# Kernel tuning notes

Hardware: AMD Instinct MI355X
Metric: run time of the kernel (lower is better)

Reference implementation:

```python
import jax, jax.numpy as jnp
import numpy as np
from jax import lax

MAX_DEG = 10
BATCH = 4096
PER_DEG = 50000              # atoms per degree bucket
N_ATOMS = PER_DEG * (MAX_DEG + 1)
F = 128                      # n_atom_features == nb_filter
EPS = 1e-5


def setup_inputs() -> dict:
    key = jax.random.key(0)
    ks = jax.random.split(key, 8)
    atoms = jax.random.normal(ks[0], (N_ATOMS, F), jnp.float32)
    # atoms sorted by degree: degree d occupies rows [d*PER_DEG, (d+1)*PER_DEG)
    deg_slice = jnp.stack([jnp.arange(MAX_DEG + 1) * PER_DEG,
                           jnp.full((MAX_DEG + 1,), PER_DEG)], axis=1).astype(jnp.int32)
    membership = jax.random.randint(ks[1], (N_ATOMS,), 0, BATCH, dtype=jnp.int32)
    inp = {"atoms": atoms, "deg_slice": deg_slice, "membership": membership}
    for d in range(1, MAX_DEG + 1):
        inp[f"adj_{d}"] = jax.random.randint(jax.random.fold_in(key, d),
                                             (PER_DEG, d), 0, N_ATOMS, dtype=jnp.int32)
    inp["W"] = jax.random.normal(ks[2], (2 * MAX_DEG + 1, F, F), jnp.float32) * 0.05
    inp["b"] = jnp.zeros((2 * MAX_DEG + 1, F), jnp.float32)
    inp["gW"] = jax.random.normal(ks[3], (MAX_DEG + 1, F, F), jnp.float32) * 0.05
    inp["gb"] = jnp.zeros((MAX_DEG + 1, F), jnp.float32)
    inp["gamma"] = jnp.ones((F,), jnp.float32)
    inp["beta"] = jnp.zeros((F,), jnp.float32)
    return inp


def reference(atoms, deg_slice, membership,
              adj_1, adj_2, adj_3, adj_4, adj_5, adj_6, adj_7, adj_8, adj_9, adj_10,
              W, b, gW, gb, gamma, beta):
    adjs = [adj_1, adj_2, adj_3, adj_4, adj_5, adj_6, adj_7, adj_8, adj_9, adj_10]
    rel_outs = [None] * (MAX_DEG + 1)
    gat_outs = [None] * (MAX_DEG + 1)
    for d in range(1, MAX_DEG + 1):
        nbr_sum = jnp.take(atoms, adjs[d - 1], axis=0).sum(axis=1)  # (PER_DEG, F)
        self_atoms = lax.dynamic_slice_in_dim(atoms, deg_slice[d, 0], PER_DEG, axis=0)
        rel_outs[d] = (nbr_sum @ W[2 * (d - 1)] + b[2 * (d - 1)]
                       + self_atoms @ W[2 * (d - 1) + 1] + b[2 * (d - 1) + 1])
        gat_outs[d] = self_atoms @ gW[d - 1] + gb[d - 1]
    # degree 0 (min_deg == 0): self transform only
    self0 = lax.dynamic_slice_in_dim(atoms, deg_slice[0, 0], PER_DEG, axis=0)
    rel_outs[0] = self0 @ W[2 * MAX_DEG] + b[2 * MAX_DEG]
    gat_outs[0] = self0 @ gW[MAX_DEG] + gb[MAX_DEG]

    activated = jnp.concatenate(rel_outs, axis=0)     # (N_ATOMS, F), degree order == atom order
    gather_atoms = jnp.concatenate(gat_outs, axis=0)  # (N_ATOMS, F)
    # graph_gather: per-molecule sum (tf.dynamic_partition + reduce_sum == segment_sum)
    graph_feat = jax.ops.segment_sum(gather_atoms, membership, num_segments=BATCH)
    # activation is 'linear' (identity); layer-norm on atom features as in call()
    m = activated.mean(axis=-1, keepdims=True)
    std = jnp.sqrt(activated.var(axis=-1, keepdims=True) + EPS)
    normed = gamma * ((activated - m) / (std + EPS)) + beta
    return normed, graph_feat
```

## Files before the change

### kernel.cpp

```cpp
#include <hip/hip_runtime.h>
#include <hip/hip_bf16.h>

#define F_DIM   128
#define PER_DEG 50000
#define NDEG    11
#define MAXD    10
#define BATCH   4096
#define N_ATOMS (PER_DEG * NDEG)

#define BM    64
#define LDST  264
#define BPD   ((PER_DEG + BM - 1) / BM)
#define WT_K  384

typedef __attribute__((ext_vector_type(4))) float f32x4;
typedef __attribute__((ext_vector_type(8))) short short8v;
typedef __attribute__((ext_vector_type(4))) short short4v;

struct AdjPtrs { const int* p[MAXD]; };

__device__ inline short bf16bits(float x) {
    __hip_bfloat16 h = __float2bfloat16(x);
    return __builtin_bit_cast(short, h);
}
__device__ inline float bf_lo(unsigned u) {
    return __builtin_bit_cast(float, u << 16);
}
__device__ inline float bf_hi(unsigned u) {
    return __builtin_bit_cast(float, u & 0xFFFF0000u);
}

__global__ void prep_wt(const float* __restrict__ W, const float* __restrict__ gW,
                        short* __restrict__ wt) {
    int idx = blockIdx.x * blockDim.x + threadIdx.x;
    const int total = NDEG * F_DIM * WT_K;
    if (idx >= total) return;
    int d   = idx / (F_DIM * WT_K);
    int rem = idx % (F_DIM * WT_K);
    int c   = rem / WT_K;
    int k   = rem % WT_K;
    float v;
    if (k < 256) {
        if (d == 0) {
            v = (k < 128) ? 0.0f : W[20 * 16384 + (k - 128) * F_DIM + c];
        } else {
            int wi = (k < 128) ? (2 * (d - 1)) : (2 * (d - 1) + 1);
            v = W[wi * 16384 + (k & 127) * F_DIM + c];
        }
    } else {
        int gidx = (d == 0) ? 10 : (d - 1);
        v = gW[gidx * 16384 + (k - 256) * F_DIM + c];
    }
    wt[idx] = bf16bits(v);
}

__global__ void to_bf16(const float* __restrict__ in, short* __restrict__ out) {
    const size_t n8 = (size_t)N_ATOMS * F_DIM / 8;
    size_t stride = (size_t)gridDim.x * blockDim.x;
    for (size_t k = (size_t)blockIdx.x * blockDim.x + threadIdx.x; k < n8; k += stride) {
        f32x4 a = ((const f32x4*)in)[2 * k];
        f32x4 c = ((const f32x4*)in)[2 * k + 1];
        short8v o = { bf16bits(a[0]), bf16bits(a[1]), bf16bits(a[2]), bf16bits(a[3]),
                      bf16bits(c[0]), bf16bits(c[1]), bf16bits(c[2]), bf16bits(c[3]) };
        ((short8v*)out)[k] = o;
    }
}

template<int GBF>
__global__ __launch_bounds__(256, 2) void fused_gc(
    const float* __restrict__ atoms,
    const short* __restrict__ abf,
    const int*   __restrict__ membership,
    AdjPtrs adj,
    const short* __restrict__ wt,
    const float* __restrict__ b,
    const float* __restrict__ gb,
    const float* __restrict__ gamma,
    const float* __restrict__ beta,
    float* __restrict__ outN,
    float* __restrict__ outG)
{
    __shared__ short As[BM * LDST];
    const int bid   = blockIdx.x;
    const int d     = bid / BPD;
    const int rb    = bid % BPD;
    const int rows0 = rb * BM;
    const int tid   = threadIdx.x;

    {
        const int rloc = tid >> 2;
        const int p    = tid & 3;
        const int grow = rows0 + rloc;
        const bool rv  = grow < PER_DEG;
        short* basep = &As[rloc * LDST + p * 32];

        if (GBF) {
            float acc[32];
            #pragma unroll
            for (int e = 0; e < 32; ++e) acc[e] = 0.0f;
            if (rv && d > 0) {
                const int* ar = adj.p[d - 1] + (size_t)grow * d;
                int idxs[MAXD];
                #pragma unroll
                for (int j = 0; j < MAXD; ++j) idxs[j] = (j < d) ? ar[j] : 0;
                #pragma unroll
                for (int j = 0; j < MAXD; ++j) {
                    if (j < d) {
                        const uint4* s = (const uint4*)(abf + (size_t)idxs[j] * F_DIM) + p * 4;
                        #pragma unroll
                        for (int q = 0; q < 4; ++q) {
                            uint4 u = s[q];
                            acc[q * 8 + 0] += bf_lo(u.x); acc[q * 8 + 1] += bf_hi(u.x);
                            acc[q * 8 + 2] += bf_lo(u.y); acc[q * 8 + 3] += bf_hi(u.y);
                            acc[q * 8 + 4] += bf_lo(u.z); acc[q * 8 + 5] += bf_hi(u.z);
                            acc[q * 8 + 6] += bf_lo(u.w); acc[q * 8 + 7] += bf_hi(u.w);
                        }
                    }
                }
            }
            #pragma unroll
            for (int q = 0; q < 4; ++q) {
                short8v nb = { bf16bits(acc[q * 8 + 0]), bf16bits(acc[q * 8 + 1]),
                               bf16bits(acc[q * 8 + 2]), bf16bits(acc[q * 8 + 3]),
                               bf16bits(acc[q * 8 + 4]), bf16bits(acc[q * 8 + 5]),
                               bf16bits(acc[q * 8 + 6]), bf16bits(acc[q * 8 + 7]) };
                *(short8v*)(basep + q * 8) = nb;
            }
            const uint4* ss = (const uint4*)(abf + (size_t)(d * PER_DEG + grow) * F_DIM) + p * 4;
            uint4 z = {0u, 0u, 0u, 0u};
            #pragma unroll
            for (int q = 0; q < 4; ++q)
                *(uint4*)(basep + 128 + q * 8) = rv ? ss[q] : z;
        } else {
            f32x4 accn[8], selfv[8];
            #pragma unroll
            for (int q = 0; q < 8; ++q) { accn[q] = 0.0f; selfv[q] = 0.0f; }
            const f32x4* atomsv = (const f32x4*)atoms;
            if (rv) {
                if (d > 0) {
                    const int* ar = adj.p[d - 1] + (size_t)grow * d;
                    int idxs[MAXD];
                    #pragma unroll
                    for (int j = 0; j < MAXD; ++j) idxs[j] = (j < d) ? ar[j] : 0;
                    #pragma unroll
                    for (int j = 0; j < MAXD; ++j) {
                        if (j < d) {
                            const f32x4* s = atomsv + (size_t)idxs[j] * 32 + p * 8;
                            #pragma unroll
                            for (int q = 0; q < 8; ++q) accn[q] += s[q];
                        }
                    }
                }
                const f32x4* s = atomsv + (size_t)(d * PER_DEG + grow) * 32 + p * 8;
                #pragma unroll
                for (int q = 0; q < 8; ++q) selfv[q] = s[q];
            }
            #pragma unroll
            for (int q = 0; q < 8; ++q) {
                short4v nb = { bf16bits(accn[q][0]),  bf16bits(accn[q][1]),
                               bf16bits(accn[q][2]),  bf16bits(accn[q][3]) };
                short4v sv = { bf16bits(selfv[q][0]), bf16bits(selfv[q][1]),
                               bf16bits(selfv[q][2]), bf16bits(selfv[q][3]) };
                *(short4v*)(basep + q * 4)       = nb;
                *(short4v*)(basep + 128 + q * 4) = sv;
            }
        }
    }
    __syncthreads();

    const int w  = tid >> 6;
    const int l  = tid & 63;
    const int cg = l & 15;
    const int rg = l >> 4;

    short8v a[8];
    const short* arow = &As[(w * 16 + cg) * LDST + rg * 8];
    #pragma unroll
    for (int s = 0; s < 8; ++s) a[s] = *(const short8v*)(arow + s * 32);

    const short* wtd = wt + (size_t)d * F_DIM * WT_K;
    f32x4 aA[8], aG[8];
    #pragma unroll
    for (int n = 0; n < 8; ++n) { aA[n] = 0.0f; aG[n] = 0.0f; }

    #pragma unroll
    for (int s = 0; s < 8; ++s) {
        #pragma unroll
        for (int n = 0; n < 8; ++n) {
            short8v bv = *(const short8v*)(wtd + (n * 16 + cg) * WT_K + s * 32 + rg * 8);
            aA[n] = __builtin_amdgcn_mfma_f32_16x16x32_bf16(a[s], bv, aA[n], 0, 0, 0);
        }
    }
    #pragma unroll
    for (int s = 0; s < 4; ++s) {
        #pragma unroll
        for (int n = 0; n < 8; ++n) {
            short8v bv = *(const short8v*)(wtd + (n * 16 + cg) * WT_K + 256 + s * 32 + rg * 8);
            aG[n] = __builtin_amdgcn_mfma_f32_16x16x32_bf16(a[4 + s], bv, aG[n], 0, 0, 0);
        }
    }

    const int gidx = (d == 0) ? 10 : (d - 1);
    float biasv[8], gbv[8], gam[8], bet[8];
    #pragma unroll
    for (int n = 0; n < 8; ++n) {
        int col = n * 16 + cg;
        biasv[n] = (d > 0) ? (b[(2 * d - 2) * F_DIM + col] + b[(2 * d - 1) * F_DIM + col])
                           : b[20 * F_DIM + col];
        gbv[n] = gb[gidx * F_DIM + col];
        gam[n] = gamma[col];
        bet[n] = beta[col];
    }
    const int valid = (PER_DEG - rows0 < BM) ? (PER_DEG - rows0) : BM;
    #pragma unroll
    for (int j = 0; j < 4; ++j) {
        const int rl = w * 16 + rg * 4 + j;
        float x[8];
        float s1 = 0.f, s2 = 0.f;
        #pragma unroll
        for (int n = 0; n < 8; ++n) {
            x[n] = aA[n][j] + biasv[n];
            s1 += x[n];
            s2 += x[n] * x[n];
        }
        #pragma unroll
        for (int m = 1; m < 16; m <<= 1) {
            s1 += __shfl_xor(s1, m);
            s2 += __shfl_xor(s2, m);
        }
        float mean = s1 * (1.0f / 128.0f);
        float var  = fmaxf(s2 * (1.0f / 128.0f) - mean * mean, 0.0f);
        float inv  = 1.0f / (sqrtf(var + 1e-5f) + 1e-5f);
        if (rl < valid) {
            const int growi = d * PER_DEG + rows0 + rl;
            float* op = outN + (size_t)growi * F_DIM;
            float* gp = outG + (size_t)membership[growi] * F_DIM;
            #pragma unroll
            for (int n = 0; n < 8; ++n) {
                int col = n * 16 + cg;
                op[col] = gam[n] * ((x[n] - mean) * inv) + bet[n];
                atomicAdd(&gp[col], aG[n][j] + gbv[n]);
            }
        }
    }
}

extern "C" void kernel_launch(void* const* d_in, const int* in_sizes, int n_in,
                              void* d_out, int out_size, void* d_ws, size_t ws_size,
                              hipStream_t stream) {
    const float* atoms      = (const float*)d_in[0];
    const int*   membership = (const int*)d_in[2];
    AdjPtrs adj;
    for (int i = 0; i < MAXD; ++i) adj.p[i] = (const int*)d_in[3 + i];
    const float* W     = (const float*)d_in[13];
    const float* b     = (const float*)d_in[14];
    const float* gW    = (const float*)d_in[15];
    const float* gb    = (const float*)d_in[16];
    const float* gamma = (const float*)d_in[17];
    const float* beta  = (const float*)d_in[18];

    float* outN = (float*)d_out;
    float* outG = outN + (size_t)N_ATOMS * F_DIM;

    const size_t wt_bytes  = (size_t)NDEG * F_DIM * WT_K * sizeof(short);
    const size_t abf_off   = (wt_bytes + 255) & ~(size_t)255;
    const size_t abf_bytes = (size_t)N_ATOMS * F_DIM * sizeof(short);
    const bool use_bf16 = ws_size >= abf_off + abf_bytes;

    short* wt = (short*)d_ws;
    const int prep_total = NDEG * F_DIM * WT_K;
    prep_wt<<<(prep_total + 255) / 256, 256, 0, stream>>>(W, gW, wt);
    hipMemsetAsync(outG, 0, (size_t)BATCH * F_DIM * sizeof(float), stream);

    if (use_bf16) {
        short* abf = (short*)((char*)d_ws + abf_off);
        to_bf16<<<2048, 256, 0, stream>>>(atoms, abf);
        fused_gc<1><<<NDEG * BPD, 256, 0, stream>>>(atoms, abf, membership, adj, wt,
                                                    b, gb, gamma, beta, outN, outG);
    } else {
        fused_gc<0><<<NDEG * BPD, 256, 0, stream>>>(atoms, nullptr, membership, adj, wt,
                                                    b, gb, gamma, beta, outN, outG);
    }
}
```

Before: 737.0 us.

## Replace per-atom gather GEMM and atomics with per-molecule sum then small GEMM

Uses linearity to move the graph gather past the matrix multiply. Atom features are first summed per (molecule, degree) bucket, using a histogram, scan and scatter to group atom indices. A small GEMM over the 1440-wide concatenated sums, with bias folded in via counts, then produces the molecule features. This removes the per-atom gather matmul and the 64M float atomicAdds from the main kernel, which now needs less LDS and targets higher occupancy. In exchange it adds several small kernels and a serial per-molecule reduction loop.

Result: faster. 619.9 us (-15.9%).

```diff
diff --git a/kernel.cpp b/kernel.cpp
--- a/kernel.cpp
+++ b/kernel.cpp
@@ -8,10 +8,13 @@
 #define BATCH   4096
 #define N_ATOMS (PER_DEG * NDEG)
 
-#define BM    64
-#define LDST  264
-#define BPD   ((PER_DEG + BM - 1) / BM)
-#define WT_K  384
+#define BM     64
+#define LDSN   136
+#define BPD    ((PER_DEG + BM - 1) / BM)
+#define WT_K   256
+#define GWT_K  1440
+#define LDST_L 264
+#define WT_K_L 384
 
 typedef __attribute__((ext_vector_type(4))) float f32x4;
 typedef __attribute__((ext_vector_type(8))) short short8v;
@@ -23,15 +26,13 @@
     __hip_bfloat16 h = __float2bfloat16(x);
     return __builtin_bit_cast(short, h);
 }
-__device__ inline float bf_lo(unsigned u) {
-    return __builtin_bit_cast(float, u << 16);
-}
-__device__ inline float bf_hi(unsigned u) {
-    return __builtin_bit_cast(float, u & 0xFFFF0000u);
-}
-
-__global__ void prep_wt(const float* __restrict__ W, const float* __restrict__ gW,
-                        short* __restrict__ wt) {
+__device__ inline float bf_lo(unsigned u) { return __builtin_bit_cast(float, u << 16); }
+__device__ inline float bf_hi(unsigned u) { return __builtin_bit_cast(float, u & 0xFFFF0000u); }
+__device__ inline float bf2f(short s) {
+    return __builtin_bit_cast(float, ((unsigned)(unsigned short)s) << 16);
+}
+
+__global__ void prep_wt_main(const float* __restrict__ W, short* __restrict__ wt) {
     int idx = blockIdx.x * blockDim.x + threadIdx.x;
     const int total = NDEG * F_DIM * WT_K;
     if (idx >= total) return;
@@ -40,18 +41,33 @@
     int c   = rem / WT_K;
     int k   = rem % WT_K;
     float v;
-    if (k < 256) {
-        if (d == 0) {
-            v = (k < 128) ? 0.0f : W[20 * 16384 + (k - 128) * F_DIM + c];
-        } else {
-            int wi = (k < 128) ? (2 * (d - 1)) : (2 * (d - 1) + 1);
-            v = W[wi * 16384 + (k & 127) * F_DIM + c];
-        }
+    if (d == 0) {
+        v = (k < 128) ? 0.0f : W[20 * 16384 + (k - 128) * F_DIM + c];
     } else {
-        int gidx = (d == 0) ? 10 : (d - 1);
-        v = gW[gidx * 16384 + (k - 256) * F_DIM + c];
+        int wi = (k < 128) ? (2 * (d - 1)) : (2 * (d - 1) + 1);
+        v = W[wi * 16384 + (k & 127) * F_DIM + c];
     }
     wt[idx] = bf16bits(v);
+}
+
+__global__ void prep_gwt(const float* __restrict__ gW, const float* __restrict__ gb,
+                         short* __restrict__ gwt) {
+    int idx = blockIdx.x * blockDim.x + threadIdx.x;
+    const int total = F_DIM * GWT_K;
+    if (idx >= total) return;
+    int c = idx / GWT_K;
+    int k = idx % GWT_K;
+    float v = 0.0f;
+    if (k < 1408) {
+        int dd = k >> 7, f = k & 127;
+        int gi = dd ? (dd - 1) : 10;
+        v = gW[gi * 16384 + f * F_DIM + c];
+    } else if (k < 1419) {
+        int dd = k - 1408;
+        int gi = dd ? (dd - 1) : 10;
+        v = gb[gi * F_DIM + c];
+    }
+    gwt[idx] = bf16bits(v);
 }
 
 __global__ void to_bf16(const float* __restrict__ in, short* __restrict__ out) {
@@ -66,21 +82,63 @@
     }
 }
 
-template<int GBF>
-__global__ __launch_bounds__(256, 2) void fused_gc(
-    const float* __restrict__ atoms,
+__global__ void hist_kernel(const int* __restrict__ mem, int* __restrict__ hist2) {
+    int i = blockIdx.x * blockDim.x + threadIdx.x;
+    if (i >= N_ATOMS) return;
+    atomicAdd(&hist2[mem[i] * NDEG + i / PER_DEG], 1);
+}
+
+__global__ void scan_offsets(const int* __restrict__ hist2,
+                             int* __restrict__ off, int* __restrict__ cur) {
+    __shared__ int lds[1024];
+    const int tid = threadIdx.x;
+    int h[4][NDEG];
+    int tsum = 0;
+    #pragma unroll
+    for (int mi = 0; mi < 4; ++mi) {
+        int m = tid * 4 + mi;
+        #pragma unroll
+        for (int dd = 0; dd < NDEG; ++dd) { h[mi][dd] = hist2[m * NDEG + dd]; tsum += h[mi][dd]; }
+    }
+    lds[tid] = tsum;
+    __syncthreads();
+    for (int ofs = 1; ofs < 1024; ofs <<= 1) {
+        int v = (tid >= ofs) ? lds[tid - ofs] : 0;
+        __syncthreads();
+        lds[tid] += v;
+        __syncthreads();
+    }
+    int run = lds[tid] - tsum;
+    #pragma unroll
+    for (int mi = 0; mi < 4; ++mi) {
+        int m = tid * 4 + mi;
+        #pragma unroll
+        for (int dd = 0; dd < NDEG; ++dd) {
+            int k = m * NDEG + dd;
+            off[k] = run; cur[k] = run;
+            run += h[mi][dd];
+        }
+    }
+}
+
+__global__ void scatter_kernel(const int* __restrict__ mem,
+                               int* __restrict__ cur, int* __restrict__ idx) {
+    int i = blockIdx.x * blockDim.x + threadIdx.x;
+    if (i >= N_ATOMS) return;
+    int pos = atomicAdd(&cur[mem[i] * NDEG + i / PER_DEG], 1);
+    idx[pos] = i;
+}
+
+__global__ __launch_bounds__(256, 4) void fused_deg(
     const short* __restrict__ abf,
-    const int*   __restrict__ membership,
     AdjPtrs adj,
     const short* __restrict__ wt,
     const float* __restrict__ b,
-    const float* __restrict__ gb,
     const float* __restrict__ gamma,
     const float* __restrict__ beta,
-    float* __restrict__ outN,
-    float* __restrict__ outG)
+    float* __restrict__ outN)
 {
-    __shared__ short As[BM * LDST];
+    __shared__ short As[BM * LDSN];
     const int bid   = blockIdx.x;
     const int d     = bid / BPD;
     const int rb    = bid % BPD;
@@ -91,9 +149,197 @@
         const int rloc = tid >> 2;
         const int p    = tid & 3;
         const int grow = rows0 + rloc;
-        const bool rv  = grow < PER_DEG;
-        short* basep = &As[rloc * LDST + p * 32];
-
+        float acc[32];
+        #pragma unroll
+        for (int e = 0; e < 32; ++e) acc[e] = 0.0f;
+        if (grow < PER_DEG && d > 0) {
+            const int* ar = adj.p[d - 1] + (size_t)grow * d;
+            int idxs[MAXD];
+            #pragma unroll
+            for (int j = 0; j < MAXD; ++j) idxs[j] = (j < d) ? ar[j] : 0;
+            #pragma unroll
+            for (int j = 0; j < MAXD; ++j) {
+                if (j < d) {
+                    const uint4* s = (const uint4*)(abf + (size_t)idxs[j] * F_DIM) + p * 4;
+                    #pragma unroll
+                    for (int q = 0; q < 4; ++q) {
+                        uint4 u = s[q];
+                        acc[q * 8 + 0] += bf_lo(u.x); acc[q * 8 + 1] += bf_hi(u.x);
+                        acc[q * 8 + 2] += bf_lo(u.y); acc[q * 8 + 3] += bf_hi(u.y);
+                        acc[q * 8 + 4] += bf_lo(u.z); acc[q * 8 + 5] += bf_hi(u.z);
+                        acc[q * 8 + 6] += bf_lo(u.w); acc[q * 8 + 7] += bf_hi(u.w);
+                    }
+                }
+            }
+        }
+        short* basep = &As[rloc * LDSN + p * 32];
+        #pragma unroll
+        for (int q = 0; q < 4; ++q) {
+            short8v nb = { bf16bits(acc[q * 8 + 0]), bf16bits(acc[q * 8 + 1]),
+                           bf16bits(acc[q * 8 + 2]), bf16bits(acc[q * 8 + 3]),
+                           bf16bits(acc[q * 8 + 4]), bf16bits(acc[q * 8 + 5]),
+                           bf16bits(acc[q * 8 + 6]), bf16bits(acc[q * 8 + 7]) };
+            *(short8v*)(basep + q * 8) = nb;
+        }
+    }
+    __syncthreads();
+
+    const int w  = tid >> 6;
+    const int l  = tid & 63;
+    const int cg = l & 15;
+    const int rg = l >> 4;
+
+    short8v a[8];
+    const short* arow = &As[(w * 16 + cg) * LDSN + rg * 8];
+    #pragma unroll
+    for (int s = 0; s < 4; ++s) a[s] = *(const short8v*)(arow + s * 32);
+    int srow = d * PER_DEG + rows0 + w * 16 + cg;
+    if (srow >= N_ATOMS) srow = N_ATOMS - 1;
+    const short* sp = abf + (size_t)srow * F_DIM + rg * 8;
+    #pragma unroll
+    for (int s = 0; s < 4; ++s) a[4 + s] = *(const short8v*)(sp + s * 32);
+
+    const short* wtd = wt + (size_t)d * F_DIM * WT_K;
+    f32x4 aA[8];
+    #pragma unroll
+    for (int n = 0; n < 8; ++n) aA[n] = 0.0f;
+    #pragma unroll
+    for (int s = 0; s < 8; ++s) {
+        #pragma unroll
+        for (int n = 0; n < 8; ++n) {
+            short8v bv = *(const short8v*)(wtd + (n * 16 + cg) * WT_K + s * 32 + rg * 8);
+            aA[n] = __builtin_amdgcn_mfma_f32_16x16x32_bf16(a[s], bv, aA[n], 0, 0, 0);
+        }
+    }
+
+    float biasv[8], gam[8], bet[8];
+    #pragma unroll
+    for (int n = 0; n < 8; ++n) {
+        int col = n * 16 + cg;
+        biasv[n] = (d > 0) ? (b[(2 * d - 2) * F_DIM + col] + b[(2 * d - 1) * F_DIM + col])
+                           : b[20 * F_DIM + col];
+        gam[n] = gamma[col];
+        bet[n] = beta[col];
+    }
+    const int valid = (PER_DEG - rows0 < BM) ? (PER_DEG - rows0) : BM;
+    #pragma unroll
+    for (int j = 0; j < 4; ++j) {
+        const int rl = w * 16 + rg * 4 + j;
+        float x[8];
+        float s1 = 0.f, s2 = 0.f;
+        #pragma unroll
+        for (int n = 0; n < 8; ++n) {
+            x[n] = aA[n][j] + biasv[n];
+            s1 += x[n];
+            s2 += x[n] * x[n];
+        }
+        #pragma unroll
+        for (int m = 1; m < 16; m <<= 1) {
+            s1 += __shfl_xor(s1, m);
+            s2 += __shfl_xor(s2, m);
+        }
+        float mean = s1 * (1.0f / 128.0f);
+        float var  = fmaxf(s2 * (1.0f / 128.0f) - mean * mean, 0.0f);
+        float inv  = 1.0f / (sqrtf(var + 1e-5f) + 1e-5f);
+        if (rl < valid) {
+            float* op = outN + (size_t)(d * PER_DEG + rows0 + rl) * F_DIM;
+            #pragma unroll
+            for (int n = 0; n < 8; ++n)
+                op[n * 16 + cg] = gam[n] * ((x[n] - mean) * inv) + bet[n];
+        }
+    }
+}
+
+__global__ __launch_bounds__(128) void mol_reduce(
+    const short* __restrict__ abf, const int* __restrict__ idx,
+    const int* __restrict__ off, const int* __restrict__ hist2,
+    short* __restrict__ sums)
+{
+    const int m = blockIdx.x;
+    const int c = threadIdx.x;
+    short* out = sums + (size_t)m * GWT_K;
+    for (int dd = 0; dd < NDEG; ++dd) {
+        const int base = off[m * NDEG + dd];
+        const int n    = hist2[m * NDEG + dd];
+        float acc = 0.0f;
+        #pragma unroll 4
+        for (int t = 0; t < n; ++t) {
+            int id = idx[base + t];
+            acc += bf2f(abf[(size_t)id * F_DIM + c]);
+        }
+        out[dd * F_DIM + c] = bf16bits(acc);
+    }
+    if (c < 32)
+        out[1408 + c] = (c < NDEG) ? bf16bits((float)hist2[m * NDEG + c]) : (short)0;
+}
+
+__global__ __launch_bounds__(256) void gat_gemm(
+    const short* __restrict__ sums, const short* __restrict__ gwt,
+    float* __restrict__ outG)
+{
+    const int rows0 = blockIdx.x * 64;
+    const int tid = threadIdx.x;
+    const int w = tid >> 6, l = tid & 63, cg = l & 15, rg = l >> 4;
+    const short* ap = sums + (size_t)(rows0 + w * 16 + cg) * GWT_K + rg * 8;
+    f32x4 acc[8];
+    #pragma unroll
+    for (int n = 0; n < 8; ++n) acc[n] = 0.0f;
+    for (int ks = 0; ks < GWT_K / 32; ++ks) {
+        short8v av = *(const short8v*)(ap + ks * 32);
+        #pragma unroll
+        for (int n = 0; n < 8; ++n) {
+            short8v bv = *(const short8v*)(gwt + (size_t)(n * 16 + cg) * GWT_K + ks * 32 + rg * 8);
+            acc[n] = __builtin_amdgcn_mfma_f32_16x16x32_bf16(av, bv, acc[n], 0, 0, 0);
+        }
+    }
+    #pragma unroll
+    for (int j = 0; j < 4; ++j) {
+        int r = rows0 + w * 16 + rg * 4 + j;
+        #pragma unroll
+        for (int n = 0; n < 8; ++n)
+            outG[(size_t)r * F_DIM + n * 16 + cg] = acc[n][j];
+    }
+}
+
+__global__ void prep_wt_full(const float* __restrict__ W, const float* __restrict__ gW,
+                             short* __restrict__ wt) {
+    int idx = blockIdx.x * blockDim.x + threadIdx.x;
+    const int total = NDEG * F_DIM * WT_K_L;
+    if (idx >= total) return;
+    int d   = idx / (F_DIM * WT_K_L);
+    int rem = idx % (F_DIM * WT_K_L);
+    int c   = rem / WT_K_L;
+    int k   = rem % WT_K_L;
+    float v;
+    if (k < 256) {
+        if (d == 0) v = (k < 128) ? 0.0f : W[20 * 16384 + (k - 128) * F_DIM + c];
+        else {
+            int wi = (k < 128) ? (2 * (d - 1)) : (2 * (d - 1) + 1);
+            v = W[wi * 16384 + (k & 127) * F_DIM + c];
+        }
+    } else {
+        int gi = (d == 0) ? 10 : (d - 1);
+        v = gW[gi * 16384 + (k - 256) * F_DIM + c];
+    }
+    wt[idx] = bf16bits(v);
+}
+
+template<int GBF>
+__global__ __launch_bounds__(256, 2) void fused_legacy(
+    const float* __restrict__ atoms, const short* __restrict__ abf,
+    const int* __restrict__ membership, AdjPtrs adj,
+    const short* __restrict__ wt, const float* __restrict__ b,
+    const float* __restrict__ gb, const float* __restrict__ gamma,
+    const float* __restrict__ beta, float* __restrict__ outN, float* __restrict__ outG)
+{
+    __shared__ short As[BM * LDST_L];
+    const int bid = blockIdx.x, d = bid / BPD, rb = bid % BPD;
+    const int rows0 = rb * BM, tid = threadIdx.x;
+    {
+        const int rloc = tid >> 2, p = tid & 3;
+        const int grow = rows0 + rloc;
+        const bool rv = grow < PER_DEG;
+        short* basep = &As[rloc * LDST_L + p * 32];
         if (GBF) {
             float acc[32];
             #pragma unroll
@@ -104,33 +350,29 @@
                 #pragma unroll
                 for (int j = 0; j < MAXD; ++j) idxs[j] = (j < d) ? ar[j] : 0;
                 #pragma unroll
-                for (int j = 0; j < MAXD; ++j) {
-                    if (j < d) {
-                        const uint4* s = (const uint4*)(abf + (size_t)idxs[j] * F_DIM) + p * 4;
-                        #pragma unroll
-                        for (int q = 0; q < 4; ++q) {
-                            uint4 u = s[q];
-                            acc[q * 8 + 0] += bf_lo(u.x); acc[q * 8 + 1] += bf_hi(u.x);
-                            acc[q * 8 + 2] += bf_lo(u.y); acc[q * 8 + 3] += bf_hi(u.y);
-                            acc[q * 8 + 4] += bf_lo(u.z); acc[q * 8 + 5] += bf_hi(u.z);
-                            acc[q * 8 + 6] += bf_lo(u.w); acc[q * 8 + 7] += bf_hi(u.w);
-                        }
+                for (int j = 0; j < MAXD; ++j) if (j < d) {
+                    const uint4* s = (const uint4*)(abf + (size_t)idxs[j] * F_DIM) + p * 4;
+                    #pragma unroll
+                    for (int q = 0; q < 4; ++q) {
+                        uint4 u = s[q];
+                        acc[q * 8 + 0] += bf_lo(u.x); acc[q * 8 + 1] += bf_hi(u.x);
+                        acc[q * 8 + 2] += bf_lo(u.y); acc[q * 8 + 3] += bf_hi(u.y);
+                        acc[q * 8 + 4] += bf_lo(u.z); acc[q * 8 + 5] += bf_hi(u.z);
+                        acc[q * 8 + 6] += bf_lo(u.w); acc[q * 8 + 7] += bf_hi(u.w);
                     }
                 }
             }
             #pragma unroll
             for (int q = 0; q < 4; ++q) {
-                short8v nb = { bf16bits(acc[q * 8 + 0]), bf16bits(acc[q * 8 + 1]),
-                               bf16bits(acc[q * 8 + 2]), bf16bits(acc[q * 8 + 3]),
-                               bf16bits(acc[q * 8 + 4]), bf16bits(acc[q * 8 + 5]),
-                               bf16bits(acc[q * 8 + 6]), bf16bits(acc[q * 8 + 7]) };
+                short8v nb = { bf16bits(acc[q*8+0]), bf16bits(acc[q*8+1]), bf16bits(acc[q*8+2]),
+                               bf16bits(acc[q*8+3]), bf16bits(acc[q*8+4]), bf16bits(acc[q*8+5]),
+                               bf16bits(acc[q*8+6]), bf16bits(acc[q*8+7]) };
                 *(short8v*)(basep + q * 8) = nb;
             }
             const uint4* ss = (const uint4*)(abf + (size_t)(d * PER_DEG + grow) * F_DIM) + p * 4;
-            uint4 z = {0u, 0u, 0u, 0u};
-            #pragma unroll
-            for (int q = 0; q < 4; ++q)
-                *(uint4*)(basep + 128 + q * 8) = rv ? ss[q] : z;
+            uint4 z = {0u,0u,0u,0u};
+            #pragma unroll
+            for (int q = 0; q < 4; ++q) *(uint4*)(basep + 128 + q * 8) = rv ? ss[q] : z;
         } else {
             f32x4 accn[8], selfv[8];
             #pragma unroll
@@ -143,12 +385,10 @@
                     #pragma unroll
                     for (int j = 0; j < MAXD; ++j) idxs[j] = (j < d) ? ar[j] : 0;
                     #pragma unroll
-                    for (int j = 0; j < MAXD; ++j) {
-                        if (j < d) {
-                            const f32x4* s = atomsv + (size_t)idxs[j] * 32 + p * 8;
-                            #pragma unroll
-                            for (int q = 0; q < 8; ++q) accn[q] += s[q];
-                        }
+                    for (int j = 0; j < MAXD; ++j) if (j < d) {
+                        const f32x4* s = atomsv + (size_t)idxs[j] * 32 + p * 8;
+                        #pragma unroll
+                        for (int q = 0; q < 8; ++q) accn[q] += s[q];
                     }
                 }
                 const f32x4* s = atomsv + (size_t)(d * PER_DEG + grow) * 32 + p * 8;
@@ -157,37 +397,30 @@
             }
             #pragma unroll
             for (int q = 0; q < 8; ++q) {
-                short4v nb = { bf16bits(accn[q][0]),  bf16bits(accn[q][1]),
-                               bf16bits(accn[q][2]),  bf16bits(accn[q][3]) };
+                short4v nb = { bf16bits(accn[q][0]), bf16bits(accn[q][1]),
+                               bf16bits(accn[q][2]), bf16bits(accn[q][3]) };
                 short4v sv = { bf16bits(selfv[q][0]), bf16bits(selfv[q][1]),
                                bf16bits(selfv[q][2]), bf16bits(selfv[q][3]) };
-                *(short4v*)(basep + q * 4)       = nb;
+                *(short4v*)(basep + q * 4) = nb;
                 *(short4v*)(basep + 128 + q * 4) = sv;
             }
         }
     }
     __syncthreads();
-
-    const int w  = tid >> 6;
-    const int l  = tid & 63;
-    const int cg = l & 15;
-    const int rg = l >> 4;
-
+    const int w = tid >> 6, l = tid & 63, cg = l & 15, rg = l >> 4;
     short8v a[8];
-    const short* arow = &As[(w * 16 + cg) * LDST + rg * 8];
+    const short* arow = &As[(w * 16 + cg) * LDST_L + rg * 8];
     #pragma unroll
     for (int s = 0; s < 8; ++s) a[s] = *(const short8v*)(arow + s * 32);
-
-    const short* wtd = wt + (size_t)d * F_DIM * WT_K;
+    const short* wtd = wt + (size_t)d * F_DIM * WT_K_L;
     f32x4 aA[8], aG[8];
     #pragma unroll
     for (int n = 0; n < 8; ++n) { aA[n] = 0.0f; aG[n] = 0.0f; }
-
     #pragma unroll
     for (int s = 0; s < 8; ++s) {
         #pragma unroll
         for (int n = 0; n < 8; ++n) {
-            short8v bv = *(const short8v*)(wtd + (n * 16 + cg) * WT_K + s * 32 + rg * 8);
+            short8v bv = *(const short8v*)(wtd + (n * 16 + cg) * WT_K_L + s * 32 + rg * 8);
             aA[n] = __builtin_amdgcn_mfma_f32_16x16x32_bf16(a[s], bv, aA[n], 0, 0, 0);
         }
     }
@@ -195,41 +428,30 @@
     for (int s = 0; s < 4; ++s) {
         #pragma unroll
         for (int n = 0; n < 8; ++n) {
-            short8v bv = *(const short8v*)(wtd + (n * 16 + cg) * WT_K + 256 + s * 32 + rg * 8);
+            short8v bv = *(const short8v*)(wtd + (n * 16 + cg) * WT_K_L + 256 + s * 32 + rg * 8);
             aG[n] = __builtin_amdgcn_mfma_f32_16x16x32_bf16(a[4 + s], bv, aG[n], 0, 0, 0);
         }
     }
-
-    const int gidx = (d == 0) ? 10 : (d - 1);
+    const int gi = (d == 0) ? 10 : (d - 1);
     float biasv[8], gbv[8], gam[8], bet[8];
     #pragma unroll
     for (int n = 0; n < 8; ++n) {
         int col = n * 16 + cg;
-        biasv[n] = (d > 0) ? (b[(2 * d - 2) * F_DIM + col] + b[(2 * d - 1) * F_DIM + col])
-                           : b[20 * F_DIM + col];
-        gbv[n] = gb[gidx * F_DIM + col];
-        gam[n] = gamma[col];
-        bet[n] = beta[col];
+        biasv[n] = (d > 0) ? (b[(2*d-2)*F_DIM+col] + b[(2*d-1)*F_DIM+col]) : b[20*F_DIM+col];
+        gbv[n] = gb[gi * F_DIM + col];
+        gam[n] = gamma[col]; bet[n] = beta[col];
     }
     const int valid = (PER_DEG - rows0 < BM) ? (PER_DEG - rows0) : BM;
     #pragma unroll
     for (int j = 0; j < 4; ++j) {
         const int rl = w * 16 + rg * 4 + j;
-        float x[8];
-        float s1 = 0.f, s2 = 0.f;
-        #pragma unroll
-        for (int n = 0; n < 8; ++n) {
-            x[n] = aA[n][j] + biasv[n];
-            s1 += x[n];
-            s2 += x[n] * x[n];
-        }
-        #pragma unroll
-        for (int m = 1; m < 16; m <<= 1) {
-            s1 += __shfl_xor(s1, m);
-            s2 += __shfl_xor(s2, m);
-        }
-        float mean = s1 * (1.0f / 128.0f);
-        float var  = fmaxf(s2 * (1.0f / 128.0f) - mean * mean, 0.0f);
+        float x[8], s1 = 0.f, s2 = 0.f;
+        #pragma unroll
+        for (int n = 0; n < 8; ++n) { x[n] = aA[n][j] + biasv[n]; s1 += x[n]; s2 += x[n]*x[n]; }
+        #pragma unroll
+        for (int m = 1; m < 16; m <<= 1) { s1 += __shfl_xor(s1, m); s2 += __shfl_xor(s2, m); }
+        float mean = s1 * (1.0f/128.0f);
+        float var  = fmaxf(s2 * (1.0f/128.0f) - mean*mean, 0.0f);
         float inv  = 1.0f / (sqrtf(var + 1e-5f) + 1e-5f);
         if (rl < valid) {
             const int growi = d * PER_DEG + rows0 + rl;
@@ -262,23 +484,48 @@
     float* outN = (float*)d_out;
     float* outG = outN + (size_t)N_ATOMS * F_DIM;
 
-    const size_t wt_bytes  = (size_t)NDEG * F_DIM * WT_K * sizeof(short);
-    const size_t abf_off   = (wt_bytes + 255) & ~(size_t)255;
-    const size_t abf_bytes = (size_t)N_ATOMS * F_DIM * sizeof(short);
-    const bool use_bf16 = ws_size >= abf_off + abf_bytes;
-
-    short* wt = (short*)d_ws;
-    const int prep_total = NDEG * F_DIM * WT_K;
-    prep_wt<<<(prep_total + 255) / 256, 256, 0, stream>>>(W, gW, wt);
-    hipMemsetAsync(outG, 0, (size_t)BATCH * F_DIM * sizeof(float), stream);
-
-    if (use_bf16) {
-        short* abf = (short*)((char*)d_ws + abf_off);
+    auto al = [](size_t x) { return (x + 255) & ~(size_t)255; };
+    const size_t sz_wt   = al((size_t)NDEG * F_DIM * WT_K * 2);
+    const size_t sz_gwt  = al((size_t)F_DIM * GWT_K * 2);
+    const size_t sz_h    = al((size_t)BATCH * NDEG * 4);
+    const size_t sz_idx  = al((size_t)N_ATOMS * 4);
+    const size_t sz_sums = al((size_t)BATCH * GWT_K * 2);
+    const size_t sz_abf  = (size_t)N_ATOMS * F_DIM * 2;
+
+    size_t o = 0;
+    short* wt    = (short*)((char*)d_ws + o); o += sz_wt;
+    short* gwt   = (short*)((char*)d_ws + o); o += sz_gwt;
+    int*   hist2 = (int*)  ((char*)d_ws + o); o += sz_h;
+    int*   offa  = (int*)  ((char*)d_ws + o); o += sz_h;
+    int*   cura  = (int*)  ((char*)d_ws + o); o += sz_h;
+    int*   idx   = (int*)  ((char*)d_ws + o); o += sz_idx;
+    short* sums  = (short*)((char*)d_ws + o); o += sz_sums;
+    short* abf   = (short*)((char*)d_ws + o); o += sz_abf;
+
+    if (ws_size >= o) {
+        prep_wt_main<<<(NDEG * F_DIM * WT_K + 255) / 256, 256, 0, stream>>>(W, wt);
+        prep_gwt<<<(F_DIM * GWT_K + 255) / 256, 256, 0, stream>>>(gW, gb, gwt);
+        hipMemsetAsync(hist2, 0, (size_t)BATCH * NDEG * 4, stream);
         to_bf16<<<2048, 256, 0, stream>>>(atoms, abf);
-        fused_gc<1><<<NDEG * BPD, 256, 0, stream>>>(atoms, abf, membership, adj, wt,
-                                                    b, gb, gamma, beta, outN, outG);
+        hist_kernel<<<(N_ATOMS + 255) / 256, 256, 0, stream>>>(membership, hist2);
+        scan_offsets<<<1, 1024, 0, stream>>>(hist2, offa, cura);
+        scatter_kernel<<<(N_ATOMS + 255) / 256, 256, 0, stream>>>(membership, cura, idx);
+        fused_deg<<<NDEG * BPD, 256, 0, stream>>>(abf, adj, wt, b, gamma, beta, outN);
+        mol_reduce<<<BATCH, 128, 0, stream>>>(abf, idx, offa, hist2, sums);
+        gat_gemm<<<BATCH / 64, 256, 0, stream>>>(sums, gwt, outG);
     } else {
-        fused_gc<0><<<NDEG * BPD, 256, 0, stream>>>(atoms, nullptr, membership, adj, wt,
-                                                    b, gb, gamma, beta, outN, outG);
-    }
-}
+        short* lwt = (short*)d_ws;
+        const size_t lwt_sz = al((size_t)NDEG * F_DIM * WT_K_L * 2);
+        prep_wt_full<<<(NDEG * F_DIM * WT_K_L + 255) / 256, 256, 0, stream>>>(W, gW, lwt);
+        hipMemsetAsync(outG, 0, (size_t)BATCH * F_DIM * 4, stream);
+        if (ws_size >= lwt_sz + sz_abf) {
+            short* abf2 = (short*)((char*)d_ws + lwt_sz);
+            to_bf16<<<2048, 256, 0, stream>>>(atoms, abf2);
+            fused_legacy<1><<<NDEG * BPD, 256, 0, stream>>>(atoms, abf2, membership, adj, lwt,
+                                                            b, gb, gamma, beta, outN, outG);
+        } else {
+            fused_legacy<0><<<NDEG * BPD, 256, 0, stream>>>(atoms, nullptr, membership, adj, lwt,
+                                                            b, gb, gamma, beta, outN, outG);
+        }
+    }
+}
```
